# Kernel optimization log

Measured on AMD Instinct MI355X. Metric: run time of the kernel, lower is better.

Reference implementation:

```python
import jax, jax.numpy as jnp
import numpy as np

N = 50000      # nodes
E = 800000     # edges (avg degree 16)
G = 64         # graphs in batch


def gcn_conv(x, edge_index, W, b):
    """PyG GCNConv: h = D^{-1/2}(A+I)D^{-1/2} (x @ W) + b, self-loops added."""
    n = x.shape[0]
    h = x @ W  # [N, out]
    loop = jnp.arange(n, dtype=edge_index.dtype)
    src = jnp.concatenate([edge_index[0], loop])
    dst = jnp.concatenate([edge_index[1], loop])
    deg = jax.ops.segment_sum(jnp.ones_like(dst, dtype=h.dtype), dst, num_segments=n)
    dinv = jnp.where(deg > 0, jax.lax.rsqrt(deg), 0.0)
    norm = dinv[src] * dinv[dst]               # [E+N]
    msg = h[src] * norm[:, None]               # gather + scale
    return jax.ops.segment_sum(msg, dst, num_segments=n) + b


def setup_inputs() -> dict:
    key = jax.random.key(0)
    ks = jax.random.split(key, 12)
    x = jax.random.normal(ks[0], (N, 512), dtype=jnp.float32)
    edge_index = jax.random.randint(ks[1], (2, E), 0, N, dtype=jnp.int64)
    batch = jnp.sort(jax.random.randint(ks[2], (N,), 0, G, dtype=jnp.int64))

    def lin(k, fin, fout):
        s = 1.0 / np.sqrt(fin)
        return jax.random.uniform(k, (fin, fout), jnp.float32, -s, s)

    return {
        "x": x, "edge_index": edge_index, "batch": batch,
        "W1": lin(ks[3], 512, 256), "b1": jnp.zeros((256,), jnp.float32),
        "W2": lin(ks[4], 256, 128), "b2": jnp.zeros((128,), jnp.float32),
        "W3": lin(ks[5], 128, 64),  "b3": jnp.zeros((64,), jnp.float32),
        "Wl": lin(ks[6], 64, 2),    "bl": jnp.zeros((2,), jnp.float32),
    }


def reference(x, edge_index, batch, W1, b1, W2, b2, W3, b3, Wl, bl):
    h = jax.nn.relu(gcn_conv(x, edge_index, W1, b1))
    h = jax.nn.relu(gcn_conv(h, edge_index, W2, b2))
    h = gcn_conv(h, edge_index, W3, b3)
    # global_mean_pool over batch ids
    sums = jax.ops.segment_sum(h, batch, num_segments=G)
    cnts = jax.ops.segment_sum(jnp.ones((h.shape[0],), h.dtype), batch, num_segments=G)
    pooled = sums / jnp.maximum(cnts, 1.0)[:, None]
    # dropout p=0.5 is identity in eval mode
    return pooled @ Wl + bl  # [G, 2]
```

## Files before the change

kernel.cpp:

```cpp
#include <hip/hip_runtime.h>
#include <hip/hip_bf16.h>


typedef __attribute__((ext_vector_type(8))) short short8_t;
typedef __attribute__((ext_vector_type(4))) float float4_t;

__device__ __forceinline__ unsigned short f2bf(float f) {
    unsigned int u = __float_as_uint(f);
    u += 0x7FFFu + ((u >> 16) & 1u);
    return (unsigned short)(u >> 16);
}
__device__ __forceinline__ float bf2f(unsigned short h) {
    return __uint_as_float(((unsigned int)h) << 16);
}

#define GLDS16(gp, lp)                                                          \
    __builtin_amdgcn_global_load_lds(                                           \
        (const __attribute__((address_space(1))) void*)(gp),                    \
        (__attribute__((address_space(3))) void*)(lp), 16, 0, 0)


__global__ __launch_bounds__(256) void conv_x_k(const float* __restrict__ x,
                                                ushort* __restrict__ Xb,
                                                int M, int Mpad) {
    int t = blockIdx.x * 256 + threadIdx.x;
    int total = Mpad * 128;
    if (t >= total) return;
    int row = t >> 7;
    ushort4 o;
    if (row < M) {
        float4 v = ((const float4*)x)[t];
        o.x = f2bf(v.x); o.y = f2bf(v.y); o.z = f2bf(v.z); o.w = f2bf(v.w);
    } else {
        o.x = o.y = o.z = o.w = 0;
    }
    ((ushort4*)Xb)[t] = o;
}

__global__ void conv_weights(const float* __restrict__ W1, ushort* __restrict__ Wt1,
                             const float* __restrict__ W2, ushort* __restrict__ Wt2,
                             const float* __restrict__ W3, ushort* __restrict__ Wt3) {
    int t = blockIdx.x * 256 + threadIdx.x;
    if (t < 131072) {
        int k = t & 511, n = t >> 9;
        Wt1[t] = f2bf(W1[(size_t)k * 256 + n]);
    } else if (t < 163840) {
        int u = t - 131072;
        int k = u & 255, n = u >> 8;
        Wt2[u] = f2bf(W2[(size_t)k * 128 + n]);
    } else if (t < 180224) {
        int u = t - 163840;
        int k = u & 127, n = u >> 7;
        Wt3[u] = (n < 64) ? f2bf(W3[(size_t)k * 64 + n]) : (ushort)0;
    }
}


__global__ void count_indeg(const int* __restrict__ dst, int* __restrict__ indeg, int E) {
    int e = blockIdx.x * blockDim.x + threadIdx.x;
    if (e < E) atomicAdd(&indeg[dst[e]], 1);
}

__global__ __launch_bounds__(1024) void scan1(const int* __restrict__ indeg,
                                              int* __restrict__ incl,
                                              int* __restrict__ part, int n) {
    __shared__ int sm[1024];
    int i = blockIdx.x * 1024 + threadIdx.x;
    int v = (i < n) ? indeg[i] : 0;
    sm[threadIdx.x] = v;
    __syncthreads();
    #pragma unroll
    for (int off = 1; off < 1024; off <<= 1) {
        int t = (threadIdx.x >= (unsigned)off) ? sm[threadIdx.x - off] : 0;
        __syncthreads();
        sm[threadIdx.x] += t;
        __syncthreads();
    }
    if (i < n) incl[i] = sm[threadIdx.x];
    if (threadIdx.x == 1023) part[blockIdx.x] = sm[1023];
}

__global__ void scan2(int* __restrict__ part, int nb) {
    int t = threadIdx.x;
    int v = (t < nb) ? part[t] : 0;
    int orig = v;
    #pragma unroll
    for (int off = 1; off < 64; off <<= 1) {
        int u = __shfl_up(v, off, 64);
        if (t >= off) v += u;
    }
    if (t < nb) part[t] = v - orig;
}

__global__ void scan3(const int* __restrict__ indeg, int* __restrict__ rowptr,
                      int* __restrict__ cursor, const int* __restrict__ part,
                      float* __restrict__ dinv, int n, int E) {
    int i = blockIdx.x * blockDim.x + threadIdx.x;
    if (i < n) {
        int excl = rowptr[i] - indeg[i] + part[i >> 10];
        rowptr[i] = excl;
        cursor[i] = excl;
        dinv[i] = rsqrtf((float)indeg[i] + 1.0f);
    }
    if (i == 0) rowptr[n] = E;
}

__global__ void fill_csr(const int* __restrict__ src, const int* __restrict__ dst,
                         int* __restrict__ cursor, int* __restrict__ col, int E) {
    int e = blockIdx.x * blockDim.x + threadIdx.x;
    if (e < E) {
        int p = atomicAdd(&cursor[dst[e]], 1);
        col[p] = src[e];
    }
}


__global__ __launch_bounds__(256) void gemm_mfma(const ushort* __restrict__ A,
                                                 const ushort* __restrict__ Bt,
                                                 const float* __restrict__ dinv,
                                                 ushort* __restrict__ C,
                                                 int M, int Ncols, int K, int ldc) {
    __shared__ __align__(16) ushort As[128 * 32];
    __shared__ __align__(16) ushort Bs[128 * 32];
    int tid = threadIdx.x;
    int lane = tid & 63, w = tid >> 6;
    int wr = w >> 1, wc = w & 1;
    int bm = blockIdx.x * 128, bn = blockIdx.y * 128;

    float4_t acc[4][4];
    #pragma unroll
    for (int i = 0; i < 4; ++i)
        #pragma unroll
        for (int j = 0; j < 4; ++j) acc[i][j] = (float4_t)0.0f;

    int r0 = tid >> 2;
    int kb = (tid & 3) * 8;
    const ushort* ga0 = A + (size_t)(bm + r0) * K + kb;
    const ushort* ga1 = A + (size_t)(bm + r0 + 64) * K + kb;
    const ushort* gb0 = Bt + (size_t)(bn + r0) * K + kb;
    const ushort* gb1 = Bt + (size_t)(bn + r0 + 64) * K + kb;
    ushort* lA0 = As + w * 512;
    ushort* lA1 = As + 2048 + w * 512;
    ushort* lB0 = Bs + w * 512;
    ushort* lB1 = Bs + 2048 + w * 512;

    int arow = wr * 64 + (lane & 15);
    int brow = wc * 64 + (lane & 15);
    int quad = lane >> 4;

    for (int k0 = 0; k0 < K; k0 += 32) {
        __syncthreads();
        GLDS16(ga0 + k0, lA0);
        GLDS16(ga1 + k0, lA1);
        GLDS16(gb0 + k0, lB0);
        GLDS16(gb1 + k0, lB1);
        __syncthreads();
        short8_t aF[4], bF[4];
        #pragma unroll
        for (int i = 0; i < 4; ++i)
            aF[i] = *(const short8_t*)&As[(arow + i * 16) * 32 + quad * 8];
        #pragma unroll
        for (int j = 0; j < 4; ++j)
            bF[j] = *(const short8_t*)&Bs[(brow + j * 16) * 32 + quad * 8];
        #pragma unroll
        for (int i = 0; i < 4; ++i)
            #pragma unroll
            for (int j = 0; j < 4; ++j)
                acc[i][j] = __builtin_amdgcn_mfma_f32_16x16x32_bf16(aF[i], bF[j], acc[i][j], 0, 0, 0);
    }

    int colb = bn + wc * 64 + (lane & 15);
    #pragma unroll
    for (int i = 0; i < 4; ++i) {
        int mb = bm + wr * 64 + i * 16 + quad * 4;
        #pragma unroll
        for (int r = 0; r < 4; ++r) {
            int m = mb + r;
            if (m >= M) continue;
            float s = dinv[m];
            #pragma unroll
            for (int j = 0; j < 4; ++j) {
                int n = colb + j * 16;
                if (n < Ncols) C[(size_t)m * ldc + n] = f2bf(acc[i][j][r] * s);
            }
        }
    }
}


template <int F, bool RELU>
__global__ __launch_bounds__(256) void agg_bf(const ushort* __restrict__ g,
                                              const int* __restrict__ rowptr,
                                              const int* __restrict__ col,
                                              const float* __restrict__ dinv,
                                              const float* __restrict__ bias,
                                              ushort* __restrict__ out,
                                              int n, int npad) {
    constexpr int VPT = F / 64;
    int wid = (int)((blockIdx.x * blockDim.x + threadIdx.x) >> 6);
    int lane = threadIdx.x & 63;
    if (wid >= npad) return;
    int off = lane * VPT;
    ushort* orow = out + (size_t)wid * F + off;
    if (wid >= n) {
        #pragma unroll
        for (int j = 0; j < VPT; ++j) orow[j] = 0;
        return;
    }
    float acc[VPT];
    #pragma unroll
    for (int j = 0; j < VPT; ++j) acc[j] = 0.f;

    int e0 = rowptr[wid];
    int deg = rowptr[wid + 1] - e0;

    for (int base = 0; base < deg; base += 64) {
        int cnt = min(64, deg - base);
        int ec = (lane < cnt) ? col[e0 + base + lane] : 0;
        int j = 0;
        for (; j + 16 <= cnt; j += 16) {
            int s[16];
            #pragma unroll
            for (int u = 0; u < 16; ++u) s[u] = __shfl(ec, j + u);
            if constexpr (VPT == 4) {
                ushort4 v[16];
                #pragma unroll
                for (int u = 0; u < 16; ++u)
                    v[u] = *(const ushort4*)(g + (size_t)s[u] * F + off);
                #pragma unroll
                for (int u = 0; u < 16; ++u) {
                    acc[0] += bf2f(v[u].x); acc[1] += bf2f(v[u].y);
                    acc[2] += bf2f(v[u].z); acc[3] += bf2f(v[u].w);
                }
            } else if constexpr (VPT == 2) {
                ushort2 v[16];
                #pragma unroll
                for (int u = 0; u < 16; ++u)
                    v[u] = *(const ushort2*)(g + (size_t)s[u] * F + off);
                #pragma unroll
                for (int u = 0; u < 16; ++u) {
                    acc[0] += bf2f(v[u].x); acc[1] += bf2f(v[u].y);
                }
            } else {
                ushort v[16];
                #pragma unroll
                for (int u = 0; u < 16; ++u) v[u] = g[(size_t)s[u] * F + off];
                #pragma unroll
                for (int u = 0; u < 16; ++u) acc[0] += bf2f(v[u]);
            }
        }
        for (; j + 4 <= cnt; j += 4) {
            int s[4];
            #pragma unroll
            for (int u = 0; u < 4; ++u) s[u] = __shfl(ec, j + u);
            if constexpr (VPT == 4) {
                ushort4 v[4];
                #pragma unroll
                for (int u = 0; u < 4; ++u)
                    v[u] = *(const ushort4*)(g + (size_t)s[u] * F + off);
                #pragma unroll
                for (int u = 0; u < 4; ++u) {
                    acc[0] += bf2f(v[u].x); acc[1] += bf2f(v[u].y);
                    acc[2] += bf2f(v[u].z); acc[3] += bf2f(v[u].w);
                }
            } else if constexpr (VPT == 2) {
                ushort2 v[4];
                #pragma unroll
                for (int u = 0; u < 4; ++u)
                    v[u] = *(const ushort2*)(g + (size_t)s[u] * F + off);
                #pragma unroll
                for (int u = 0; u < 4; ++u) {
                    acc[0] += bf2f(v[u].x); acc[1] += bf2f(v[u].y);
                }
            } else {
                ushort v[4];
                #pragma unroll
                for (int u = 0; u < 4; ++u) v[u] = g[(size_t)s[u] * F + off];
                #pragma unroll
                for (int u = 0; u < 4; ++u) acc[0] += bf2f(v[u]);
            }
        }
        for (; j < cnt; ++j) {
            int s = __shfl(ec, j);
            const ushort* row = g + (size_t)s * F + off;
            if constexpr (VPT == 4) {
                ushort4 v = *(const ushort4*)row;
                acc[0] += bf2f(v.x); acc[1] += bf2f(v.y);
                acc[2] += bf2f(v.z); acc[3] += bf2f(v.w);
            } else if constexpr (VPT == 2) {
                ushort2 v = *(const ushort2*)row;
                acc[0] += bf2f(v.x); acc[1] += bf2f(v.y);
            } else {
                acc[0] += bf2f(row[0]);
            }
        }
    }

    const ushort* rowi = g + (size_t)wid * F + off;
    float di = dinv[wid];
    #pragma unroll
    for (int j = 0; j < VPT; ++j) {
        float v = di * (acc[j] + bf2f(rowi[j])) + bias[off + j];
        if (RELU) v = fmaxf(v, 0.f);
        orow[j] = f2bf(v);
    }
}


__global__ __launch_bounds__(256) void pool_sorted(const ushort* __restrict__ h,
                                                   const int* __restrict__ batch,
                                                   float* __restrict__ sums,
                                                   float* __restrict__ cnt, int n) {
    int wave = (int)((blockIdx.x * blockDim.x + threadIdx.x) >> 6);
    int lane = threadIdx.x & 63;
    int start = wave * 64;
    if (start >= n) return;
    int end = min(start + 64, n);
    float acc = 0.f;
    int cur = batch[start];
    int runlen = 0;
    for (int i = start; i < end; ++i) {
        int b = batch[i];
        if (b != cur) {
            atomicAdd(&sums[cur * 64 + lane], acc);
            if (lane == 0) atomicAdd(&cnt[cur], (float)runlen);
            acc = 0.f;
            runlen = 0;
            cur = b;
        }
        acc += bf2f(h[(size_t)i * 64 + lane]);
        runlen++;
    }
    atomicAdd(&sums[cur * 64 + lane], acc);
    if (lane == 0) atomicAdd(&cnt[cur], (float)runlen);
}

__global__ void final_lin(const float* __restrict__ sums, const float* __restrict__ cnt,
                          const float* __restrict__ Wl, const float* __restrict__ bl,
                          float* __restrict__ out) {
    int t = threadIdx.x;
    int g = t >> 1, j = t & 1;
    float c = fmaxf(cnt[g], 1.0f);
    float a = 0.f;
    #pragma unroll
    for (int k = 0; k < 64; ++k) a += sums[g * 64 + k] * Wl[k * 2 + j];
    out[t] = a / c + bl[j];
}


extern "C" void kernel_launch(void* const* d_in, const int* in_sizes, int n_in,
                              void* d_out, int out_size, void* d_ws, size_t ws_size,
                              hipStream_t stream) {
    const float* x   = (const float*)d_in[0];
    const int*   ei  = (const int*)d_in[1];
    const int*   bat = (const int*)d_in[2];
    const float* W1  = (const float*)d_in[3];
    const float* b1  = (const float*)d_in[4];
    const float* W2  = (const float*)d_in[5];
    const float* b2  = (const float*)d_in[6];
    const float* W3  = (const float*)d_in[7];
    const float* b3  = (const float*)d_in[8];
    const float* Wl  = (const float*)d_in[9];
    const float* bl  = (const float*)d_in[10];
    float* out = (float*)d_out;

    const int N = in_sizes[0] / 512;
    const int E = in_sizes[1] / 2;
    const int Mpad = ((N + 127) / 128) * 128;
    const int* src = ei;
    const int* dst = ei + E;

    char* w = (char*)d_ws;
    auto alloc = [&](size_t bytes) {
        char* p = w;
        w += (bytes + 255) & ~(size_t)255;
        return p;
    };
    ushort* Xb   = (ushort*)alloc((size_t)Mpad * 512 * 2);
    ushort* G    = (ushort*)alloc((size_t)Mpad * 256 * 2);
    ushort* H    = (ushort*)alloc((size_t)Mpad * 256 * 2);
    ushort* Wt1  = (ushort*)alloc(256 * 512 * 2);
    ushort* Wt2  = (ushort*)alloc(128 * 256 * 2);
    ushort* Wt3  = (ushort*)alloc(128 * 128 * 2);
    float* dinv  = (float*)alloc((size_t)N * 4);
    int* rowptr  = (int*)alloc((size_t)(N + 1) * 4);
    int* cursor  = (int*)alloc((size_t)N * 4);
    int* col     = (int*)alloc((size_t)E * 4);
    int* part    = (int*)alloc(256 * 4);
    size_t zbytes = (size_t)N * 4 + 64 * 64 * 4 + 64 * 4;
    int* indeg   = (int*)alloc(zbytes);
    float* sums  = (float*)(indeg + N);
    float* cnt   = sums + 64 * 64;

    hipMemsetAsync(indeg, 0, zbytes, stream);

    conv_x_k<<<(Mpad * 128 + 255) / 256, 256, 0, stream>>>(x, Xb, N, Mpad);
    conv_weights<<<(180224 + 255) / 256, 256, 0, stream>>>(W1, Wt1, W2, Wt2, W3, Wt3);

    count_indeg<<<(E + 255) / 256, 256, 0, stream>>>(dst, indeg, E);
    int nb = (N + 1023) / 1024;
    scan1<<<nb, 1024, 0, stream>>>(indeg, rowptr, part, N);
    scan2<<<1, 64, 0, stream>>>(part, nb);
    scan3<<<(N + 255) / 256, 256, 0, stream>>>(indeg, rowptr, cursor, part, dinv, N, E);
    fill_csr<<<(E + 255) / 256, 256, 0, stream>>>(src, dst, cursor, col, E);

    int npad = Mpad;
    gemm_mfma<<<dim3(Mpad / 128, 2), 256, 0, stream>>>(Xb, Wt1, dinv, G, N, 256, 512, 256);
    agg_bf<256, true><<<npad / 4, 256, 0, stream>>>(G, rowptr, col, dinv, b1, H, N, npad);
    gemm_mfma<<<dim3(Mpad / 128, 1), 256, 0, stream>>>(H, Wt2, dinv, G, N, 128, 256, 128);
    agg_bf<128, true><<<npad / 4, 256, 0, stream>>>(G, rowptr, col, dinv, b2, H, N, npad);
    gemm_mfma<<<dim3(Mpad / 128, 1), 256, 0, stream>>>(H, Wt3, dinv, G, N, 64, 128, 64);
    agg_bf<64, false><<<npad / 4, 256, 0, stream>>>(G, rowptr, col, dinv, b3, H, N, npad);

    pool_sorted<<<(N + 255) / 256, 256, 0, stream>>>(H, bat, sums, cnt, N);
    final_lin<<<1, 128, 0, stream>>>(sums, cnt, Wl, bl, out);
}
```

Measured before the change: 493.8 us.

## Double-buffer GEMM LDS loads and unify SpMM gather tail with masked FMA

The GEMM now keeps two LDS buffers and issues the global-to-LDS DMA for the next K slice before running MFMAs on the current one, so load latency overlaps with compute. The SpMM aggregation drops its 4-wide and scalar remainder loops. It always gathers 16 neighbors and masks out-of-range ones with a zero-weight FMA, which gives uniform, deeply unrolled loads at the cost of some wasted gathers. Those masked gathers read row 0 (lanes past cnt hold ec=0), which is valid memory. The GEMM loop assumes K is a multiple of 64, which holds for 512, 256 and 128.

Result: no change. 488.7 us (-1.0%).

```diff
diff --git a/kernel.cpp b/kernel.cpp
--- a/kernel.cpp
+++ b/kernel.cpp
@@ -115,13 +115,31 @@
 }
 
 
+__device__ __forceinline__ void mfma_step(const ushort* __restrict__ Asb,
+                                          const ushort* __restrict__ Bsb,
+                                          int arow, int brow, int quad,
+                                          float4_t (&acc)[4][4]) {
+    short8_t aF[4], bF[4];
+    #pragma unroll
+    for (int i = 0; i < 4; ++i)
+        aF[i] = *(const short8_t*)&Asb[(arow + i * 16) * 32 + quad * 8];
+    #pragma unroll
+    for (int j = 0; j < 4; ++j)
+        bF[j] = *(const short8_t*)&Bsb[(brow + j * 16) * 32 + quad * 8];
+    #pragma unroll
+    for (int i = 0; i < 4; ++i)
+        #pragma unroll
+        for (int j = 0; j < 4; ++j)
+            acc[i][j] = __builtin_amdgcn_mfma_f32_16x16x32_bf16(aF[i], bF[j], acc[i][j], 0, 0, 0);
+}
+
 __global__ __launch_bounds__(256) void gemm_mfma(const ushort* __restrict__ A,
                                                  const ushort* __restrict__ Bt,
                                                  const float* __restrict__ dinv,
                                                  ushort* __restrict__ C,
                                                  int M, int Ncols, int K, int ldc) {
-    __shared__ __align__(16) ushort As[128 * 32];
-    __shared__ __align__(16) ushort Bs[128 * 32];
+    __shared__ __align__(16) ushort As[2 * 4096];
+    __shared__ __align__(16) ushort Bs[2 * 4096];
     int tid = threadIdx.x;
     int lane = tid & 63, w = tid >> 6;
     int wr = w >> 1, wc = w & 1;
@@ -139,35 +157,30 @@
     const ushort* ga1 = A + (size_t)(bm + r0 + 64) * K + kb;
     const ushort* gb0 = Bt + (size_t)(bn + r0) * K + kb;
     const ushort* gb1 = Bt + (size_t)(bn + r0 + 64) * K + kb;
-    ushort* lA0 = As + w * 512;
-    ushort* lA1 = As + 2048 + w * 512;
-    ushort* lB0 = Bs + w * 512;
-    ushort* lB1 = Bs + 2048 + w * 512;
+    int w512 = w * 512;
+
+#define ISSUE_DMA(kk, bufofs)                              \
+    do {                                                   \
+        GLDS16(ga0 + (kk), As + (bufofs) + w512);          \
+        GLDS16(ga1 + (kk), As + (bufofs) + 2048 + w512);   \
+        GLDS16(gb0 + (kk), Bs + (bufofs) + w512);          \
+        GLDS16(gb1 + (kk), Bs + (bufofs) + 2048 + w512);   \
+    } while (0)
 
     int arow = wr * 64 + (lane & 15);
     int brow = wc * 64 + (lane & 15);
     int quad = lane >> 4;
 
-    for (int k0 = 0; k0 < K; k0 += 32) {
+    ISSUE_DMA(0, 0);
+    for (int k0 = 0; k0 < K; k0 += 64) {
         __syncthreads();
-        GLDS16(ga0 + k0, lA0);
-        GLDS16(ga1 + k0, lA1);
-        GLDS16(gb0 + k0, lB0);
-        GLDS16(gb1 + k0, lB1);
+        ISSUE_DMA(k0 + 32, 4096);
+        mfma_step(As, Bs, arow, brow, quad, acc);
         __syncthreads();
-        short8_t aF[4], bF[4];
-        #pragma unroll
-        for (int i = 0; i < 4; ++i)
-            aF[i] = *(const short8_t*)&As[(arow + i * 16) * 32 + quad * 8];
-        #pragma unroll
-        for (int j = 0; j < 4; ++j)
-            bF[j] = *(const short8_t*)&Bs[(brow + j * 16) * 32 + quad * 8];
-        #pragma unroll
-        for (int i = 0; i < 4; ++i)
-            #pragma unroll
-            for (int j = 0; j < 4; ++j)
-                acc[i][j] = __builtin_amdgcn_mfma_f32_16x16x32_bf16(aF[i], bF[j], acc[i][j], 0, 0, 0);
-    }
+        if (k0 + 64 < K) ISSUE_DMA(k0 + 64, 0);
+        mfma_step(As + 4096, Bs + 4096, arow, brow, quad, acc);
+    }
+#undef ISSUE_DMA
 
     int colb = bn + wc * 64 + (lane & 15);
     #pragma unroll
@@ -217,8 +230,7 @@
     for (int base = 0; base < deg; base += 64) {
         int cnt = min(64, deg - base);
         int ec = (lane < cnt) ? col[e0 + base + lane] : 0;
-        int j = 0;
-        for (; j + 16 <= cnt; j += 16) {
+        for (int j = 0; j < cnt; j += 16) {
             int s[16];
             #pragma unroll
             for (int u = 0; u < 16; ++u) s[u] = __shfl(ec, j + u);
@@ -229,8 +241,11 @@
                     v[u] = *(const ushort4*)(g + (size_t)s[u] * F + off);
                 #pragma unroll
                 for (int u = 0; u < 16; ++u) {
-                    acc[0] += bf2f(v[u].x); acc[1] += bf2f(v[u].y);
-                    acc[2] += bf2f(v[u].z); acc[3] += bf2f(v[u].w);
+                    float wv = (j + u < cnt) ? 1.f : 0.f;
+                    acc[0] = fmaf(wv, bf2f(v[u].x), acc[0]);
+                    acc[1] = fmaf(wv, bf2f(v[u].y), acc[1]);
+                    acc[2] = fmaf(wv, bf2f(v[u].z), acc[2]);
+                    acc[3] = fmaf(wv, bf2f(v[u].w), acc[3]);
                 }
             } else if constexpr (VPT == 2) {
                 ushort2 v[16];
@@ -239,59 +254,19 @@
                     v[u] = *(const ushort2*)(g + (size_t)s[u] * F + off);
                 #pragma unroll
                 for (int u = 0; u < 16; ++u) {
-                    acc[0] += bf2f(v[u].x); acc[1] += bf2f(v[u].y);
+                    float wv = (j + u < cnt) ? 1.f : 0.f;
+                    acc[0] = fmaf(wv, bf2f(v[u].x), acc[0]);
+                    acc[1] = fmaf(wv, bf2f(v[u].y), acc[1]);
                 }
             } else {
                 ushort v[16];
                 #pragma unroll
                 for (int u = 0; u < 16; ++u) v[u] = g[(size_t)s[u] * F + off];
                 #pragma unroll
-                for (int u = 0; u < 16; ++u) acc[0] += bf2f(v[u]);
-            }
-        }
-        for (; j + 4 <= cnt; j += 4) {
-            int s[4];
-            #pragma unroll
-            for (int u = 0; u < 4; ++u) s[u] = __shfl(ec, j + u);
-            if constexpr (VPT == 4) {
-                ushort4 v[4];
-                #pragma unroll
-                for (int u = 0; u < 4; ++u)
-                    v[u] = *(const ushort4*)(g + (size_t)s[u] * F + off);
-                #pragma unroll
-                for (int u = 0; u < 4; ++u) {
-                    acc[0] += bf2f(v[u].x); acc[1] += bf2f(v[u].y);
-                    acc[2] += bf2f(v[u].z); acc[3] += bf2f(v[u].w);
+                for (int u = 0; u < 16; ++u) {
+                    float wv = (j + u < cnt) ? 1.f : 0.f;
+                    acc[0] = fmaf(wv, bf2f(v[u]), acc[0]);
                 }
-            } else if constexpr (VPT == 2) {
-                ushort2 v[4];
-                #pragma unroll
-                for (int u = 0; u < 4; ++u)
-                    v[u] = *(const ushort2*)(g + (size_t)s[u] * F + off);
-                #pragma unroll
-                for (int u = 0; u < 4; ++u) {
-                    acc[0] += bf2f(v[u].x); acc[1] += bf2f(v[u].y);
-                }
-            } else {
-                ushort v[4];
-                #pragma unroll
-                for (int u = 0; u < 4; ++u) v[u] = g[(size_t)s[u] * F + off];
-                #pragma unroll
-                for (int u = 0; u < 4; ++u) acc[0] += bf2f(v[u]);
-            }
-        }
-        for (; j < cnt; ++j) {
-            int s = __shfl(ec, j);
-            const ushort* row = g + (size_t)s * F + off;
-            if constexpr (VPT == 4) {
-                ushort4 v = *(const ushort4*)row;
-                acc[0] += bf2f(v.x); acc[1] += bf2f(v.y);
-                acc[2] += bf2f(v.z); acc[3] += bf2f(v.w);
-            } else if constexpr (VPT == 2) {
-                ushort2 v = *(const ushort2*)row;
-                acc[0] += bf2f(v.x); acc[1] += bf2f(v.y);
-            } else {
-                acc[0] += bf2f(row[0]);
             }
         }
     }
```
